# Optimization experiments

Hardware: AMD Instinct MI355X
Metric: run time of the kernel (lower is better)

## Reference

```python
import jax, jax.numpy as jnp
import numpy as np

DIM, HIDDEN, E = 1024, 4096, 8
B, L = 2, 2048


def setup_inputs() -> dict:
    key = jax.random.key(0)
    ks = jax.random.split(key, 6)
    s_in = 1.0 / np.sqrt(DIM)
    s_h = 1.0 / np.sqrt(HIDDEN)
    return {
        "x": jax.random.normal(ks[0], (B, L, DIM), dtype=jnp.float32),
        "Wg": jax.random.uniform(ks[1], (E, DIM), jnp.float32, -s_in, s_in),
        "W1": jax.random.uniform(ks[2], (E, DIM, HIDDEN), jnp.float32, -s_in, s_in),
        "b1": jax.random.uniform(ks[3], (E, HIDDEN), jnp.float32, -s_in, s_in),
        "W2": jax.random.uniform(ks[4], (E, HIDDEN, DIM), jnp.float32, -s_h, s_h),
        "b2": jax.random.uniform(ks[5], (E, DIM), jnp.float32, -s_h, s_h),
    }


def reference(x, Wg, W1, b1, W2, b2):
    # Router: top-1 over gate logits (softmax is monotone, argmax of probs == argmax of logits)
    gate_logits = jnp.einsum("bld,ed->ble", x, Wg)  # [B, L, E]
    top1 = jnp.argmax(gate_logits, axis=-1)          # [B, L] int
    out = jnp.zeros_like(x)
    # Fixed small loop over experts (structurally distinct weights); per-expert
    # dense MLP + select, honoring top-1 dispatch/combine semantics.
    for e in range(E):
        mask = (top1 == e)[..., None]                                   # [B, L, 1]
        h = jax.nn.gelu(jnp.einsum("bld,dh->blh", x, W1[e]) + b1[e],
                        approximate=False)                              # [B, L, H]
        y = jnp.einsum("blh,hd->bld", h, W2[e]) + b2[e]                 # [B, L, D]
        out = jnp.where(mask, y, out)
    return out
```

## Files before the change

### kernel.cpp

```cpp
#include <hip/hip_runtime.h>
#include <hip/hip_bf16.h>
#include <math.h>

#define NTOK 4096
#define DIMSZ 1024
#define HID 4096
#define NE 8
#define RT_MAX 40

typedef unsigned short u16;
typedef unsigned int u32;
typedef __attribute__((ext_vector_type(8))) short bf16x8;
typedef __attribute__((ext_vector_type(4))) float f32x4;

static __device__ __forceinline__ u16 f2bf(float f) {
    u32 u = __float_as_uint(f);
    u32 r = u + 0x7fffu + ((u >> 16) & 1u);
    return (u16)(r >> 16);
}

static __device__ __forceinline__ u32 pk2bf(float lo, float hi) {
    __hip_bfloat162 h = __float22bfloat162_rn(make_float2(lo, hi));
    return *(u32*)&h;
}

__global__ void k_init(int* counts, int* cursor) {
    if (threadIdx.x < NE) { counts[threadIdx.x] = 0; cursor[threadIdx.x] = 0; }
}

__global__ __launch_bounds__(256) void k_router(const float* __restrict__ x,
                                                const float* __restrict__ Wg,
                                                int* __restrict__ ids,
                                                int* __restrict__ counts) {
    int wave = threadIdx.x >> 6;
    int lane = threadIdx.x & 63;
    int t = blockIdx.x * 4 + wave;

    const float4* xr = (const float4*)(x + (size_t)t * DIMSZ);
    float4 xv[4];
#pragma unroll
    for (int j = 0; j < 4; j++) xv[j] = xr[j * 64 + lane];

    float s[NE];
#pragma unroll
    for (int e = 0; e < NE; e++) {
        const float4* wr = (const float4*)(Wg + (size_t)e * DIMSZ);
        float p = 0.f;
#pragma unroll
        for (int j = 0; j < 4; j++) {
            float4 w = wr[j * 64 + lane];
            p += xv[j].x * w.x + xv[j].y * w.y + xv[j].z * w.z + xv[j].w * w.w;
        }
#pragma unroll
        for (int m = 32; m >= 1; m >>= 1) p += __shfl_xor(p, m, 64);
        s[e] = p;
    }
    if (lane == 0) {
        int best = 0;
#pragma unroll
        for (int e = 1; e < NE; e++) if (s[e] > s[best]) best = e;
        ids[t] = best;
        atomicAdd(&counts[best], 1);
    }
}

__global__ void k_scan(const int* __restrict__ counts, int* __restrict__ offs) {
    if (threadIdx.x == 0) {
        int a = 0;
        for (int e = 0; e < NE; e++) { offs[e] = a; a += counts[e]; }
    }
}

__global__ __launch_bounds__(256) void k_gather(const float* __restrict__ x,
                                                const int* __restrict__ ids,
                                                const int* __restrict__ offs,
                                                int* __restrict__ cursor,
                                                int* __restrict__ perm,
                                                u16* __restrict__ Xg) {
    int t = blockIdx.x;
    __shared__ int sp;
    if (threadIdx.x == 0) {
        int e = ids[t];
        int p = offs[e] + atomicAdd(&cursor[e], 1);
        perm[p] = t;
        sp = p;
    }
    __syncthreads();
    int p = sp;
    const float4* src = (const float4*)(x + (size_t)t * DIMSZ);
    float4 v = src[threadIdx.x];
    u32 w0 = pk2bf(v.x, v.y);
    u32 w1 = pk2bf(v.z, v.w);
    uint2* dst = (uint2*)(Xg + (size_t)p * DIMSZ + threadIdx.x * 4);
    *dst = make_uint2(w0, w1);
}

template <int KDIM, int NDIM, int EPI>
__global__ __launch_bounds__(256) void k_gemm(const u16* __restrict__ A,
                                              const float* __restrict__ Ball,
                                              const float* __restrict__ biasAll,
                                              const int* __restrict__ counts,
                                              const int* __restrict__ offs,
                                              const int* __restrict__ perm,
                                              u16* __restrict__ Hout,
                                              float* __restrict__ Fout) {
    constexpr int NT = NDIM / 128;
    constexpr int NWG = RT_MAX * NT;
    constexpr int CPX = NWG / 8;
    int bid = blockIdx.x;
    int wid = (bid & 7) * CPX + (bid >> 3);
    int x = wid % RT_MAX;
    int n0 = (wid / RT_MAX) * 128;

    int e = -1, lrt = 0, a0 = 0;
#pragma unroll
    for (int i = 0; i < NE; i++) {
        int rt = (counts[i] + 127) >> 7;
        if (e < 0 && x < a0 + rt) { e = i; lrt = x - a0; }
        a0 += rt;
    }
    if (e < 0) return;
    int row0 = offs[e] + lrt * 128;
    int nrows = offs[e] + counts[e] - row0;
    if (nrows > 128) nrows = 128;

    __shared__ alignas(16) u16 As[128][64];
    __shared__ alignas(16) u16 Bs[128][64];

    int tid = threadIdx.x;
    int lane = tid & 63;
    int wave = tid >> 6;
    int wr = wave >> 1, wc = wave & 1;

    const u16* srcA[4];
#pragma unroll
    for (int p = 0; p < 4; p++) {
        int g = p * 256 + tid;
        int r = g >> 3, slot = g & 7;
        int rc = r < nrows ? r : nrows - 1;
        srcA[p] = A + (size_t)(row0 + rc) * KDIM + ((slot ^ (r & 7)) * 8);
    }
    int bn4 = (tid & 31) * 4;
    int bkb = tid >> 5;
    const float* srcB = Ball + (size_t)e * KDIM * NDIM + (size_t)(bkb * 8) * NDIM + n0 + bn4;

    f32x4 acc[4][4] = {};
    int fr = lane & 15, fc = lane >> 4;

    for (int kk = 0; kk < KDIM / 64; kk++) {
        __syncthreads();
#pragma unroll
        for (int p = 0; p < 4; p++) {
            __builtin_amdgcn_global_load_lds(
                (const __attribute__((address_space(1))) void*)(srcA[p] + kk * 64),
                (__attribute__((address_space(3))) void*)((u16*)&As[0][0] + (p * 256 + wave * 64) * 8),
                16, 0, 0);
        }
        {
            const float* bp = srcB + (size_t)kk * 64 * NDIM;
            float4 v[8];
#pragma unroll
            for (int j = 0; j < 8; j++) v[j] = *(const float4*)(bp + (size_t)j * NDIM);
            const float* vf = (const float*)v;
#pragma unroll
            for (int i = 0; i < 4; i++) {
                int N = bn4 + i;
                u32 w0 = pk2bf(vf[0 + i],  vf[4 + i]);
                u32 w1 = pk2bf(vf[8 + i],  vf[12 + i]);
                u32 w2 = pk2bf(vf[16 + i], vf[20 + i]);
                u32 w3 = pk2bf(vf[24 + i], vf[28 + i]);
                u32 off = (u32)(bkb * 16) ^ (u32)((N & 7) << 4);
                *(uint4*)((char*)&Bs[N][0] + off) = make_uint4(w0, w1, w2, w3);
            }
        }
        __syncthreads();
#pragma unroll
        for (int k2 = 0; k2 < 2; k2++) {
            bf16x8 af[4], bfr[4];
#pragma unroll
            for (int m = 0; m < 4; m++) {
                int r = wr * 64 + m * 16 + fr;
                u32 off = (u32)(k2 * 64 + fc * 16) ^ (u32)((r & 7) << 4);
                af[m] = *(const bf16x8*)((const char*)&As[r][0] + off);
            }
#pragma unroll
            for (int n = 0; n < 4; n++) {
                int N = wc * 64 + n * 16 + fr;
                u32 off = (u32)(k2 * 64 + fc * 16) ^ (u32)((N & 7) << 4);
                bfr[n] = *(const bf16x8*)((const char*)&Bs[N][0] + off);
            }
#pragma unroll
            for (int m = 0; m < 4; m++)
#pragma unroll
                for (int n = 0; n < 4; n++)
                    acc[m][n] = __builtin_amdgcn_mfma_f32_16x16x32_bf16(af[m], bfr[n], acc[m][n], 0, 0, 0);
        }
    }

    int cb = lane & 15;
    int rq = lane >> 4;
#pragma unroll
    for (int m = 0; m < 4; m++) {
        int rbase = wr * 64 + m * 16 + rq * 4;
#pragma unroll
        for (int n = 0; n < 4; n++) {
            int col = n0 + wc * 64 + n * 16 + cb;
            float bias = biasAll[(size_t)e * NDIM + col];
#pragma unroll
            for (int j = 0; j < 4; j++) {
                int r = rbase + j;
                if (r < nrows) {
                    float v = acc[m][n][j] + bias;
                    int p = row0 + r;
                    if (EPI == 1) {
                        float g = 0.5f * v * (1.0f + erff(v * 0.70710678118654752f));
                        Hout[(size_t)p * NDIM + col] = f2bf(g);
                    } else {
                        int trow = perm[p];
                        Fout[(size_t)trow * NDIM + col] = v;
                    }
                }
            }
        }
    }
}

extern "C" void kernel_launch(void* const* d_in, const int* in_sizes, int n_in,
                              void* d_out, int out_size, void* d_ws, size_t ws_size,
                              hipStream_t stream) {
    const float* x  = (const float*)d_in[0];
    const float* Wg = (const float*)d_in[1];
    const float* W1 = (const float*)d_in[2];
    const float* b1 = (const float*)d_in[3];
    const float* W2 = (const float*)d_in[4];
    const float* b2 = (const float*)d_in[5];
    float* out = (float*)d_out;

    char* ws = (char*)d_ws;
    int* ids    = (int*)(ws + 0);
    int* counts = (int*)(ws + 16384);
    int* offs   = (int*)(ws + 16448);
    int* cursor = (int*)(ws + 16512);
    int* perm   = (int*)(ws + 16576);
    u16* Xg     = (u16*)(ws + 33024);
    u16* H      = (u16*)(ws + 33024 + 8388608);

    k_init<<<dim3(1), dim3(64), 0, stream>>>(counts, cursor);
    k_router<<<dim3(NTOK / 4), dim3(256), 0, stream>>>(x, Wg, ids, counts);
    k_scan<<<dim3(1), dim3(64), 0, stream>>>(counts, offs);
    k_gather<<<dim3(NTOK), dim3(256), 0, stream>>>(x, ids, offs, cursor, perm, Xg);
    k_gemm<DIMSZ, HID, 1><<<dim3(RT_MAX * (HID / 128)), dim3(256), 0, stream>>>(
        Xg, W1, b1, counts, offs, perm, H, (float*)nullptr);
    k_gemm<HID, DIMSZ, 2><<<dim3(RT_MAX * (DIMSZ / 128)), dim3(256), 0, stream>>>(
        H, W2, b2, counts, offs, perm, (u16*)nullptr, out);
}
```

Baseline: 345.2 us.

## Double-buffer LDS tiles to overlap next-tile loads with MFMA compute

Splits the A and B shared-memory tiles into two buffers. The loads for tile k+1 (A via global_load_lds, B into registers) are issued before the MFMAs on tile k, and B is converted and written to the other buffer afterwards, so each iteration needs one barrier instead of two. This is meant to hide global-memory latency behind compute. In exchange it doubles LDS use to 64KB per block, which can lower occupancy, and adds register pressure from the prefetched B values.

```diff
diff --git a/kernel.cpp b/kernel.cpp
--- a/kernel.cpp
+++ b/kernel.cpp
@@ -107,6 +107,7 @@
     constexpr int NT = NDIM / 128;
     constexpr int NWG = RT_MAX * NT;
     constexpr int CPX = NWG / 8;
+    constexpr int NK = KDIM / 64;
     int bid = blockIdx.x;
     int wid = (bid & 7) * CPX + (bid >> 3);
     int x = wid % RT_MAX;
@@ -124,8 +125,8 @@
     int nrows = offs[e] + counts[e] - row0;
     if (nrows > 128) nrows = 128;
 
-    __shared__ alignas(16) u16 As[128][64];
-    __shared__ alignas(16) u16 Bs[128][64];
+    __shared__ alignas(16) u16 As[2][128][64];
+    __shared__ alignas(16) u16 Bs[2][128][64];
 
     int tid = threadIdx.x;
     int lane = tid & 63;
@@ -147,33 +148,52 @@
     f32x4 acc[4][4] = {};
     int fr = lane & 15, fc = lane >> 4;
 
-    for (int kk = 0; kk < KDIM / 64; kk++) {
-        __syncthreads();
-#pragma unroll
-        for (int p = 0; p < 4; p++) {
-            __builtin_amdgcn_global_load_lds(
-                (const __attribute__((address_space(1))) void*)(srcA[p] + kk * 64),
-                (__attribute__((address_space(3))) void*)((u16*)&As[0][0] + (p * 256 + wave * 64) * 8),
-                16, 0, 0);
-        }
-        {
-            const float* bp = srcB + (size_t)kk * 64 * NDIM;
-            float4 v[8];
-#pragma unroll
-            for (int j = 0; j < 8; j++) v[j] = *(const float4*)(bp + (size_t)j * NDIM);
-            const float* vf = (const float*)v;
-#pragma unroll
-            for (int i = 0; i < 4; i++) {
-                int N = bn4 + i;
-                u32 w0 = pk2bf(vf[0 + i],  vf[4 + i]);
-                u32 w1 = pk2bf(vf[8 + i],  vf[12 + i]);
-                u32 w2 = pk2bf(vf[16 + i], vf[20 + i]);
-                u32 w3 = pk2bf(vf[24 + i], vf[28 + i]);
-                u32 off = (u32)(bkb * 16) ^ (u32)((N & 7) << 4);
-                *(uint4*)((char*)&Bs[N][0] + off) = make_uint4(w0, w1, w2, w3);
-            }
-        }
-        __syncthreads();
+    float4 breg[8];
+
+#define LOAD_B(KK)                                                              \
+    {                                                                           \
+        const float* bp = srcB + (size_t)(KK) * 64 * NDIM;                      \
+        _Pragma("unroll")                                                       \
+        for (int j = 0; j < 8; j++) breg[j] = *(const float4*)(bp + (size_t)j * NDIM); \
+    }
+
+#define STAGE_A(BUF, KK)                                                        \
+    {                                                                           \
+        _Pragma("unroll")                                                       \
+        for (int p = 0; p < 4; p++) {                                           \
+            __builtin_amdgcn_global_load_lds(                                   \
+                (const __attribute__((address_space(1))) void*)(srcA[p] + (KK) * 64), \
+                (__attribute__((address_space(3))) void*)((u16*)&As[BUF][0][0] + (p * 256 + wave * 64) * 8), \
+                16, 0, 0);                                                      \
+        }                                                                       \
+    }
+
+#define WRITE_B(BUF)                                                            \
+    {                                                                           \
+        const float* vf = (const float*)breg;                                   \
+        _Pragma("unroll")                                                       \
+        for (int i = 0; i < 4; i++) {                                           \
+            int N = bn4 + i;                                                    \
+            u32 w0 = pk2bf(vf[0 + i],  vf[4 + i]);                              \
+            u32 w1 = pk2bf(vf[8 + i],  vf[12 + i]);                             \
+            u32 w2 = pk2bf(vf[16 + i], vf[20 + i]);                             \
+            u32 w3 = pk2bf(vf[24 + i], vf[28 + i]);                             \
+            u32 off = (u32)(bkb * 16) ^ (u32)((N & 7) << 4);                    \
+            *(uint4*)((char*)&Bs[BUF][N][0] + off) = make_uint4(w0, w1, w2, w3); \
+        }                                                                       \
+    }
+
+    LOAD_B(0);
+    STAGE_A(0, 0);
+    WRITE_B(0);
+    __syncthreads();
+
+    for (int kk = 0; kk < NK; kk++) {
+        int cur = kk & 1;
+        if (kk + 1 < NK) {
+            LOAD_B(kk + 1);
+            STAGE_A(cur ^ 1, kk + 1);
+        }
 #pragma unroll
         for (int k2 = 0; k2 < 2; k2++) {
             bf16x8 af[4], bfr[4];
@@ -181,13 +201,13 @@
             for (int m = 0; m < 4; m++) {
                 int r = wr * 64 + m * 16 + fr;
                 u32 off = (u32)(k2 * 64 + fc * 16) ^ (u32)((r & 7) << 4);
-                af[m] = *(const bf16x8*)((const char*)&As[r][0] + off);
+                af[m] = *(const bf16x8*)((const char*)&As[cur][r][0] + off);
             }
 #pragma unroll
             for (int n = 0; n < 4; n++) {
                 int N = wc * 64 + n * 16 + fr;
                 u32 off = (u32)(k2 * 64 + fc * 16) ^ (u32)((N & 7) << 4);
-                bfr[n] = *(const bf16x8*)((const char*)&Bs[N][0] + off);
+                bfr[n] = *(const bf16x8*)((const char*)&Bs[cur][N][0] + off);
             }
 #pragma unroll
             for (int m = 0; m < 4; m++)
@@ -195,7 +215,14 @@
                 for (int n = 0; n < 4; n++)
                     acc[m][n] = __builtin_amdgcn_mfma_f32_16x16x32_bf16(af[m], bfr[n], acc[m][n], 0, 0, 0);
         }
-    }
+        if (kk + 1 < NK) {
+            WRITE_B(cur ^ 1);
+            __syncthreads();
+        }
+    }
+#undef LOAD_B
+#undef STAGE_A
+#undef WRITE_B
 
     int cb = lane & 15;
     int rq = lane >> 4;
```

Measured after the change: 380.3 us. 10.2% more time.

## Pre-transpose weights to bf16, triple-buffer async GEMM loads, split-K second GEMM

Applied to the files above, without the earlier changes.

A new pre-pass kernel converts W1/W2 to bf16 and transposes them, so both GEMM operands can be streamed straight into LDS with async global_load_lds. The main loop becomes a three-stage pipeline over K=32 slices with explicit vmcnt waits and barriers. The second GEMM is split along K into two halves that accumulate into a zeroed output with atomics, which adds parallelism. The cost is an extra full pass over the fp32 weights each call, plus atomic traffic and a zeroing kernel.

```diff
diff --git a/kernel.cpp b/kernel.cpp
--- a/kernel.cpp
+++ b/kernel.cpp
@@ -13,6 +13,8 @@
 typedef __attribute__((ext_vector_type(8))) short bf16x8;
 typedef __attribute__((ext_vector_type(4))) float f32x4;
 
+#define SWZ(r) (((r) >> 1) & 3)
+
 static __device__ __forceinline__ u16 f2bf(float f) {
     u32 u = __float_as_uint(f);
     u32 r = u + 0x7fffu + ((u >> 16) & 1u);
@@ -26,6 +28,11 @@
 
 __global__ void k_init(int* counts, int* cursor) {
     if (threadIdx.x < NE) { counts[threadIdx.x] = 0; cursor[threadIdx.x] = 0; }
+}
+
+__global__ void k_zero(float* p) {
+    int i = blockIdx.x * 1024 + threadIdx.x * 4;
+    *(float4*)(p + i) = make_float4(0.f, 0.f, 0.f, 0.f);
 }
 
 __global__ __launch_bounds__(256) void k_router(const float* __restrict__ x,
@@ -95,22 +102,76 @@
     *dst = make_uint2(w0, w1);
 }
 
-template <int KDIM, int NDIM, int EPI>
-__global__ __launch_bounds__(256) void k_gemm(const u16* __restrict__ A,
-                                              const float* __restrict__ Ball,
-                                              const float* __restrict__ biasAll,
-                                              const int* __restrict__ counts,
-                                              const int* __restrict__ offs,
-                                              const int* __restrict__ perm,
-                                              u16* __restrict__ Hout,
-                                              float* __restrict__ Fout) {
+__global__ __launch_bounds__(256) void k_wt(const float* __restrict__ W1,
+                                            const float* __restrict__ W2,
+                                            u16* __restrict__ W1T,
+                                            u16* __restrict__ W2T) {
+    int bid = blockIdx.x;
+    const float* src;
+    u16* dst;
+    int K, N, kt, nt;
+    if (bid < 8192) {
+        int e = bid >> 10, t = bid & 1023;
+        kt = t >> 6; nt = t & 63;
+        src = W1 + (size_t)e * 1024 * 4096;
+        dst = W1T + (size_t)e * 4096 * 1024;
+        K = 1024; N = 4096;
+    } else {
+        int b = bid - 8192;
+        int e = b >> 10, t = b & 1023;
+        kt = t >> 4; nt = t & 15;
+        src = W2 + (size_t)e * 4096 * 1024;
+        dst = W2T + (size_t)e * 1024 * 4096;
+        K = 4096; N = 1024;
+    }
+    __shared__ u32 T[32][65];
+    int tid = threadIdx.x;
+#pragma unroll
+    for (int pass = 0; pass < 2; pass++) {
+        int kp = (tid >> 4) + pass * 16;
+        int nc = (tid & 15) * 4;
+        const float* r0 = src + (size_t)(kt * 64 + 2 * kp) * N + nt * 64 + nc;
+        float4 a = *(const float4*)r0;
+        float4 b = *(const float4*)(r0 + N);
+        T[kp][nc + 0] = pk2bf(a.x, b.x);
+        T[kp][nc + 1] = pk2bf(a.y, b.y);
+        T[kp][nc + 2] = pk2bf(a.z, b.z);
+        T[kp][nc + 3] = pk2bf(a.w, b.w);
+    }
+    __syncthreads();
+    int n = tid >> 2;
+    int sb = (tid & 3) * 8;
+    u16* orow = dst + (size_t)(nt * 64 + n) * K + kt * 64;
+#pragma unroll
+    for (int p = 0; p < 2; p++) {
+        int s = sb + p * 4;
+        uint4 w = make_uint4(T[s][n], T[s + 1][n], T[s + 2][n], T[s + 3][n]);
+        *(uint4*)(orow + 2 * s) = w;
+    }
+}
+
+template <int KDIM, int NDIM, int EPI, int KSPLIT>
+__global__ __launch_bounds__(256, 3) void k_gemm(const u16* __restrict__ A,
+                                                 const u16* __restrict__ Wt,
+                                                 const float* __restrict__ biasAll,
+                                                 const int* __restrict__ counts,
+                                                 const int* __restrict__ offs,
+                                                 const int* __restrict__ perm,
+                                                 u16* __restrict__ Hout,
+                                                 float* __restrict__ Fout) {
     constexpr int NT = NDIM / 128;
-    constexpr int NWG = RT_MAX * NT;
+    constexpr int NREST = NT * KSPLIT;
+    constexpr int NWG = RT_MAX * NREST;
     constexpr int CPX = NWG / 8;
+    constexpr int KL = KDIM / KSPLIT;
+    constexpr int NKL = KL / 32;
     int bid = blockIdx.x;
     int wid = (bid & 7) * CPX + (bid >> 3);
-    int x = wid % RT_MAX;
-    int n0 = (wid / RT_MAX) * 128;
+    int x = wid / NREST;
+    int rest = wid % NREST;
+    int ks = rest % KSPLIT;
+    int n0 = (rest / KSPLIT) * 128;
+    int kbase = ks * KL;
 
     int e = -1, lrt = 0, a0 = 0;
 #pragma unroll
@@ -124,78 +185,98 @@
     int nrows = offs[e] + counts[e] - row0;
     if (nrows > 128) nrows = 128;
 
-    __shared__ alignas(16) u16 As[128][64];
-    __shared__ alignas(16) u16 Bs[128][64];
+    __shared__ alignas(16) u16 Asb[3][128][32];
+    __shared__ alignas(16) u16 Bsb[3][128][32];
 
     int tid = threadIdx.x;
     int lane = tid & 63;
     int wave = tid >> 6;
     int wr = wave >> 1, wc = wave & 1;
 
-    const u16* srcA[4];
-#pragma unroll
-    for (int p = 0; p < 4; p++) {
+    const u16* srcA[2];
+    const u16* srcB[2];
+#pragma unroll
+    for (int p = 0; p < 2; p++) {
         int g = p * 256 + tid;
-        int r = g >> 3, slot = g & 7;
+        int r = g >> 2, slot = g & 3;
         int rc = r < nrows ? r : nrows - 1;
-        srcA[p] = A + (size_t)(row0 + rc) * KDIM + ((slot ^ (r & 7)) * 8);
-    }
-    int bn4 = (tid & 31) * 4;
-    int bkb = tid >> 5;
-    const float* srcB = Ball + (size_t)e * KDIM * NDIM + (size_t)(bkb * 8) * NDIM + n0 + bn4;
+        int kg = (slot ^ SWZ(r)) * 8;
+        srcA[p] = A + (size_t)(row0 + rc) * KDIM + kbase + kg;
+        srcB[p] = Wt + (size_t)e * NDIM * KDIM + (size_t)(n0 + r) * KDIM + kbase + kg;
+    }
 
     f32x4 acc[4][4] = {};
     int fr = lane & 15, fc = lane >> 4;
 
-    for (int kk = 0; kk < KDIM / 64; kk++) {
-        __syncthreads();
-#pragma unroll
-        for (int p = 0; p < 4; p++) {
-            __builtin_amdgcn_global_load_lds(
-                (const __attribute__((address_space(1))) void*)(srcA[p] + kk * 64),
-                (__attribute__((address_space(3))) void*)((u16*)&As[0][0] + (p * 256 + wave * 64) * 8),
-                16, 0, 0);
-        }
-        {
-            const float* bp = srcB + (size_t)kk * 64 * NDIM;
-            float4 v[8];
-#pragma unroll
-            for (int j = 0; j < 8; j++) v[j] = *(const float4*)(bp + (size_t)j * NDIM);
-            const float* vf = (const float*)v;
-#pragma unroll
-            for (int i = 0; i < 4; i++) {
-                int N = bn4 + i;
-                u32 w0 = pk2bf(vf[0 + i],  vf[4 + i]);
-                u32 w1 = pk2bf(vf[8 + i],  vf[12 + i]);
-                u32 w2 = pk2bf(vf[16 + i], vf[20 + i]);
-                u32 w3 = pk2bf(vf[24 + i], vf[28 + i]);
-                u32 off = (u32)(bkb * 16) ^ (u32)((N & 7) << 4);
-                *(uint4*)((char*)&Bs[N][0] + off) = make_uint4(w0, w1, w2, w3);
-            }
-        }
-        __syncthreads();
-#pragma unroll
-        for (int k2 = 0; k2 < 2; k2++) {
-            bf16x8 af[4], bfr[4];
-#pragma unroll
-            for (int m = 0; m < 4; m++) {
-                int r = wr * 64 + m * 16 + fr;
-                u32 off = (u32)(k2 * 64 + fc * 16) ^ (u32)((r & 7) << 4);
-                af[m] = *(const bf16x8*)((const char*)&As[r][0] + off);
-            }
-#pragma unroll
-            for (int n = 0; n < 4; n++) {
-                int N = wc * 64 + n * 16 + fr;
-                u32 off = (u32)(k2 * 64 + fc * 16) ^ (u32)((N & 7) << 4);
-                bfr[n] = *(const bf16x8*)((const char*)&Bs[N][0] + off);
-            }
-#pragma unroll
-            for (int m = 0; m < 4; m++)
-#pragma unroll
-                for (int n = 0; n < 4; n++)
-                    acc[m][n] = __builtin_amdgcn_mfma_f32_16x16x32_bf16(af[m], bfr[n], acc[m][n], 0, 0, 0);
-        }
-    }
+    u16 *A0 = &Asb[0][0][0], *A1 = &Asb[1][0][0], *A2 = &Asb[2][0][0];
+    u16 *B0 = &Bsb[0][0][0], *B1 = &Bsb[1][0][0], *B2 = &Bsb[2][0][0];
+
+#define STAGE(AD, BD, KT)                                                       \
+    {                                                                           \
+        _Pragma("unroll")                                                       \
+        for (int p = 0; p < 2; p++) {                                           \
+            __builtin_amdgcn_global_load_lds(                                   \
+                (const __attribute__((address_space(1))) void*)(srcA[p] + (size_t)(KT) * 32), \
+                (__attribute__((address_space(3))) void*)((AD) + (p * 256 + wave * 64) * 8), \
+                16, 0, 0);                                                      \
+            __builtin_amdgcn_global_load_lds(                                   \
+                (const __attribute__((address_space(1))) void*)(srcB[p] + (size_t)(KT) * 32), \
+                (__attribute__((address_space(3))) void*)((BD) + (p * 256 + wave * 64) * 8), \
+                16, 0, 0);                                                      \
+        }                                                                       \
+    }
+
+#define COMPUTE(AP, BP)                                                         \
+    {                                                                           \
+        bf16x8 af[4], bfr[4];                                                   \
+        _Pragma("unroll")                                                       \
+        for (int m = 0; m < 4; m++) {                                           \
+            int r = wr * 64 + m * 16 + fr;                                      \
+            af[m] = *(const bf16x8*)((AP) + r * 32 + (fc ^ SWZ(r)) * 8);        \
+        }                                                                       \
+        _Pragma("unroll")                                                       \
+        for (int n = 0; n < 4; n++) {                                           \
+            int N = wc * 64 + n * 16 + fr;                                      \
+            bfr[n] = *(const bf16x8*)((BP) + N * 32 + (fc ^ SWZ(N)) * 8);       \
+        }                                                                       \
+        _Pragma("unroll")                                                       \
+        for (int m = 0; m < 4; m++)                                             \
+            _Pragma("unroll")                                                   \
+            for (int n = 0; n < 4; n++)                                         \
+                acc[m][n] = __builtin_amdgcn_mfma_f32_16x16x32_bf16(af[m], bfr[n], acc[m][n], 0, 0, 0); \
+    }
+
+#define WAITV(N) asm volatile("s_waitcnt vmcnt(" #N ")" ::: "memory")
+#define BAR()    __builtin_amdgcn_s_barrier()
+#define SBAR()   __builtin_amdgcn_sched_barrier(0)
+
+    STAGE(A0, B0, 0);
+    STAGE(A1, B1, 1);
+
+    for (int kk = 0; kk < NKL - 2; kk++) {
+        WAITV(4);
+        BAR();
+        SBAR();
+        STAGE(A2, B2, kk + 2);
+        COMPUTE(A0, B0);
+        u16* t;
+        t = A0; A0 = A1; A1 = A2; A2 = t;
+        t = B0; B0 = B1; B1 = B2; B2 = t;
+    }
+    WAITV(4);
+    BAR();
+    SBAR();
+    COMPUTE(A0, B0);
+    WAITV(0);
+    BAR();
+    SBAR();
+    COMPUTE(A1, B1);
+
+#undef STAGE
+#undef COMPUTE
+#undef WAITV
+#undef BAR
+#undef SBAR
 
     int cb = lane & 15;
     int rq = lane >> 4;
@@ -205,7 +286,7 @@
 #pragma unroll
         for (int n = 0; n < 4; n++) {
             int col = n0 + wc * 64 + n * 16 + cb;
-            float bias = biasAll[(size_t)e * NDIM + col];
+            float bias = (EPI == 2 && ks != 0) ? 0.f : biasAll[(size_t)e * NDIM + col];
 #pragma unroll
             for (int j = 0; j < 4; j++) {
                 int r = rbase + j;
@@ -217,7 +298,7 @@
                         Hout[(size_t)p * NDIM + col] = f2bf(g);
                     } else {
                         int trow = perm[p];
-                        Fout[(size_t)trow * NDIM + col] = v;
+                        atomicAdd(&Fout[(size_t)trow * NDIM + col], v);
                     }
                 }
             }
@@ -242,15 +323,20 @@
     int* offs   = (int*)(ws + 16448);
     int* cursor = (int*)(ws + 16512);
     int* perm   = (int*)(ws + 16576);
-    u16* Xg     = (u16*)(ws + 33024);
-    u16* H      = (u16*)(ws + 33024 + 8388608);
+
+    u16* Xg   = (u16*)(ws + 65536);
+    u16* H    = (u16*)(ws + 65536 + 8388608);
+    u16* W1T  = (u16*)(ws + 65536 + 8388608 + 33554432);
+    u16* W2T  = (u16*)(ws + 65536 + 8388608 + 33554432 + 67108864);
 
     k_init<<<dim3(1), dim3(64), 0, stream>>>(counts, cursor);
     k_router<<<dim3(NTOK / 4), dim3(256), 0, stream>>>(x, Wg, ids, counts);
     k_scan<<<dim3(1), dim3(64), 0, stream>>>(counts, offs);
     k_gather<<<dim3(NTOK), dim3(256), 0, stream>>>(x, ids, offs, cursor, perm, Xg);
-    k_gemm<DIMSZ, HID, 1><<<dim3(RT_MAX * (HID / 128)), dim3(256), 0, stream>>>(
-        Xg, W1, b1, counts, offs, perm, H, (float*)nullptr);
-    k_gemm<HID, DIMSZ, 2><<<dim3(RT_MAX * (DIMSZ / 128)), dim3(256), 0, stream>>>(
-        H, W2, b2, counts, offs, perm, (u16*)nullptr, out);
-}
+    k_wt<<<dim3(16384), dim3(256), 0, stream>>>(W1, W2, W1T, W2T);
+    k_zero<<<dim3(NTOK * DIMSZ / 1024), dim3(256), 0, stream>>>(out);
+    k_gemm<DIMSZ, HID, 1, 1><<<dim3(RT_MAX * (HID / 128)), dim3(256), 0, stream>>>(
+        Xg, W1T, b1, counts, offs, perm, H, (float*)nullptr);
+    k_gemm<HID, DIMSZ, 2, 2><<<dim3(RT_MAX * (DIMSZ / 128) * 2), dim3(256), 0, stream>>>(
+        H, W2T, b2, counts, offs, perm, (u16*)nullptr, out);
+}
```

After: 365.7 us. 1.06x slower.
